# Performance work log

Hardware: AMD Instinct MI355X
Metric: run time of the kernel (lower is better)

## Reference

```python
import jax, jax.numpy as jnp
import numpy as np

B, S, E, H = 4, 1024, 1024, 16
HD = E // H
MAX_SEQ = 5000


def setup_inputs() -> dict:
    key = jax.random.key(0)
    ks = jax.random.split(key, 10)
    def lin(kw, kb):
        w = jax.random.normal(kw, (E, E), dtype=jnp.float32) * (1.0 / np.sqrt(E))
        b = jax.random.normal(kb, (E,), dtype=jnp.float32) * 0.01
        return w, b
    wq, bq = lin(ks[0], ks[1])
    wk, bk = lin(ks[2], ks[3])
    wv, bv = lin(ks[4], ks[5])
    wo, bo = lin(ks[6], ks[7])
    rpe_table = jax.random.normal(ks[8], (H, 2 * MAX_SEQ - 1, HD), dtype=jnp.float32) * 0.02
    x = jax.random.normal(ks[9], (B, S, E), dtype=jnp.float32)
    return {"x": x, "wq": wq, "bq": bq, "wk": wk, "bk": bk,
            "wv": wv, "bv": bv, "wo": wo, "bo": bo, "rpe_table": rpe_table}


def reference(x, wq, bq, wk, bk, wv, bv, wo, bo, rpe_table):
    b, s, e = x.shape
    scale = 1.0 / np.sqrt(HD)
    # projections (torch Linear: y = x @ W^T + b), reshape to (b, h, s, hd)
    q = (x @ wq.T + bq).reshape(b, s, H, HD).transpose(0, 2, 1, 3)
    k = (x @ wk.T + bk).reshape(b, s, H, HD).transpose(0, 2, 1, 3)
    v = (x @ wv.T + bv).reshape(b, s, H, HD).transpose(0, 2, 1, 3)
    scores = jnp.einsum('bhqd,bhkd->bhqk', q, k) * scale
    # RPE: rpe[h, q, k, d] = table[h, q - k + s - 1, d]; factor the einsum:
    # rel[b,h,q,r] = sum_d q[b,h,q,d] * table[h,r,d], then gather r = q - k + s - 1
    table = rpe_table[:, : 2 * s - 1]               # (H, 2s-1, HD)
    rel = jnp.einsum('bhqd,hrd->bhqr', q, table)    # (b, H, s, 2s-1)
    idx = jnp.arange(s)[:, None] - jnp.arange(s)[None, :] + (s - 1)  # (s, s)
    rpe_scores = jnp.take_along_axis(
        rel, jnp.broadcast_to(idx[None, None], (b, H, s, s)), axis=-1)
    attn = jax.nn.softmax(scores + rpe_scores, axis=-1)
    ctx = jnp.einsum('bhqk,bhkd->bhqd', attn, v)
    ctx = ctx.transpose(0, 2, 1, 3).reshape(b, s, e)
    return ctx @ wo.T + bo
```

## Files before the change

kernel.cpp:

```cpp
#include <hip/hip_runtime.h>
#include <hip/hip_bf16.h>
#include <stdint.h>

typedef __attribute__((ext_vector_type(8))) short s8v;
typedef __attribute__((ext_vector_type(4))) float f32x4;
typedef __attribute__((ext_vector_type(16))) float f32x16;

union V16 { uint4 u4; unsigned int u[4]; s8v s; };

__device__ inline s8v u4_to_s8(uint4 v) { V16 c; c.u4 = v; return c.s; }
__device__ inline s8v words_to_s8(unsigned int a, unsigned int b, unsigned int c, unsigned int d) {
  V16 t; t.u[0] = a; t.u[1] = b; t.u[2] = c; t.u[3] = d; return t.s;
}
__device__ inline unsigned short f2b(float f) {
  __hip_bfloat16 h = __float2bfloat16(f);
  unsigned short u; __builtin_memcpy(&u, &h, 2); return u;
}
__device__ inline unsigned int pack2(float lo, float hi) {
  return ((unsigned int)f2b(hi) << 16) | (unsigned int)f2b(lo);
}
__device__ inline unsigned int cvtpk(float lo, float hi) {
  unsigned int r; asm("v_cvt_pk_bf16_f32 %0, %1, %2" : "=v"(r) : "v"(lo), "v"(hi)); return r;
}
__device__ inline float exp2_fast(float x) {
#if __has_builtin(__builtin_amdgcn_exp2f)
  return __builtin_amdgcn_exp2f(x);
#else
  float y; asm("v_exp_f32 %0, %1" : "=v"(y) : "v"(x)); return y;
#endif
}
__device__ inline void gld16(const void* g, void* lds) {
  __builtin_amdgcn_global_load_lds((const __attribute__((address_space(1))) void*)g,
                                   (__attribute__((address_space(3))) void*)lds, 16, 0, 0);
}

#define LOG2E 1.4426950408889634f

__global__ void cvt_fused_kernel(const float* __restrict__ x, const float* __restrict__ wq,
                                 const float* __restrict__ wk, const float* __restrict__ wv,
                                 const float* __restrict__ wo, const float* __restrict__ tb,
                                 __hip_bfloat16* __restrict__ XB, __hip_bfloat16* __restrict__ WQKV,
                                 __hip_bfloat16* __restrict__ WOb, __hip_bfloat16* __restrict__ TBL) {
  const int bid = blockIdx.x;
  if (bid < 4096) {
    size_t i = ((size_t)bid * 256 + threadIdx.x) * 8;
    const float* src; __hip_bfloat16* dst; size_t off;
    if (i < 4194304)      { src = x;  dst = XB;             off = i; }
    else if (i < 5242880) { src = wq; dst = WQKV;           off = i - 4194304; }
    else if (i < 6291456) { src = wk; dst = WQKV + 1048576; off = i - 5242880; }
    else if (i < 7340032) { src = wv; dst = WQKV + 2097152; off = i - 6291456; }
    else                  { src = wo; dst = WOb;            off = i - 7340032; }
    const float4* s4 = (const float4*)(src + off);
    float4 a = s4[0], b = s4[1];
    uint4 o;
    o.x = pack2(a.x, a.y); o.y = pack2(a.z, a.w);
    o.z = pack2(b.x, b.y); o.w = pack2(b.z, b.w);
    *(uint4*)(dst + off) = o;
  } else {
    size_t i = ((size_t)(bid - 4096) * 256 + threadIdx.x) * 8;
    int h = (int)(i >> 17);
    int rem = (int)(i & 131071);
    int r = rem >> 6, c = rem & 63;
    uint4 o;
    if (r < 2047) {
      const float4* s4 = (const float4*)(tb + ((size_t)h * 9999 + r) * 64 + c);
      float4 a = s4[0], b = s4[1];
      o.x = pack2(a.x * LOG2E, a.y * LOG2E); o.y = pack2(a.z * LOG2E, a.w * LOG2E);
      o.z = pack2(b.x * LOG2E, b.y * LOG2E); o.w = pack2(b.z * LOG2E, b.w * LOG2E);
    } else { o.x = 0u; o.y = 0u; o.z = 0u; o.w = 0u; }
    *(uint4*)(TBL + i) = o;
  }
}

__global__ __launch_bounds__(256, 3) void gemm_qkv(
    const __hip_bfloat16* __restrict__ A,
    const __hip_bfloat16* __restrict__ Bt,
    const float* __restrict__ bq, const float* __restrict__ bk, const float* __restrict__ bv,
    __hip_bfloat16* __restrict__ QB, __hip_bfloat16* __restrict__ KB,
    __hip_bfloat16* __restrict__ VTB) {
  __shared__ __align__(16) char smem[32768];
  char* As = smem;
  char* Bs = smem + 16384;
  const int tid = threadIdx.x;
  const int w = tid >> 6, l = tid & 63;
  const int wr = w >> 1, wc = w & 1;
  const int lr = l & 15, lg = l >> 4;
  const int m0 = blockIdx.y * 128, n0 = blockIdx.x * 128;

  f32x4 acc[4][4] = {};

  for (int kt = 0; kt < 16; ++kt) {
    __syncthreads();
    #pragma unroll
    for (int i = 0; i < 4; ++i) {
      const int off = i * 4096 + w * 1024;
      const int loff = off + l * 16;
      const int row = loff >> 7;
      const int cb = loff & 127;
      const int sc = cb ^ ((row & 7) << 4);
      gld16((const char*)A  + (size_t)(m0 + row) * 2048 + kt * 128 + sc, As + off);
      gld16((const char*)Bt + (size_t)(n0 + row) * 2048 + kt * 128 + sc, Bs + off);
    }
    asm volatile("s_waitcnt vmcnt(0)" ::: "memory");
    __syncthreads();
    #pragma unroll
    for (int ks = 0; ks < 2; ++ks) {
      uint4 af[4], bf4[4];
      #pragma unroll
      for (int i = 0; i < 4; ++i) {
        const int ra = wr * 64 + i * 16 + lr;
        const int rb = wc * 64 + i * 16 + lr;
        const int cb = ks * 64 + lg * 16;
        af[i]  = *(const uint4*)(As + ra * 128 + (cb ^ ((ra & 7) << 4)));
        bf4[i] = *(const uint4*)(Bs + rb * 128 + (cb ^ ((rb & 7) << 4)));
      }
      #pragma unroll
      for (int i = 0; i < 4; ++i) {
        #pragma unroll
        for (int j = 0; j < 4; ++j)
          acc[i][j] = __builtin_amdgcn_mfma_f32_16x16x32_bf16(u4_to_s8(af[i]), u4_to_s8(bf4[j]), acc[i][j], 0, 0, 0);
      }
    }
  }

  const int mrow = m0 + wr * 64 + lg * 4;
  const int ncol = n0 + wc * 64 + lr;
  const int cls = blockIdx.x >> 3;

  if (cls < 2) {
    const float sc = cls ? 0.125f * LOG2E : 1.0f;
    const float* bias = cls ? bk : bq;
    __hip_bfloat16* op = cls ? KB : QB;
    #pragma unroll
    for (int j = 0; j < 4; ++j) {
      const int n = ncol - cls * 1024 + j * 16;
      const float bia = bias[n];
      const int hh = n >> 6, hd = n & 63;
      #pragma unroll
      for (int i = 0; i < 4; ++i) {
        #pragma unroll
        for (int r = 0; r < 4; ++r) {
          const int m = mrow + i * 16 + r;
          const int bb = m >> 10, ss = m & 1023;
          op[(((size_t)(bb * 16 + hh)) * 1024 + ss) * 64 + hd] = __float2bfloat16((acc[i][j][r] + bia) * sc);
        }
      }
    }
  } else {
    #pragma unroll
    for (int j = 0; j < 4; ++j) {
      const int f = ncol - 2048 + j * 16;
      const float bia = bv[f];
      const int fh = f >> 6, fd = f & 63;
      #pragma unroll
      for (int i = 0; i < 4; ++i) {
        const int m = mrow + i * 16;
        const int bb = m >> 10, ss = m & 1023;
        ushort4 qv;
        qv.x = f2b(acc[i][j][0] + bia); qv.y = f2b(acc[i][j][1] + bia);
        qv.z = f2b(acc[i][j][2] + bia); qv.w = f2b(acc[i][j][3] + bia);
        *(ushort4*)((char*)VTB + (((size_t)bb * 1048576 + (size_t)fh * 65536 + fd * 1024 + ss) * 2)) = qv;
      }
    }
  }
}

__global__ __launch_bounds__(256, 3) void gemm_out(
    const __hip_bfloat16* __restrict__ A,
    const __hip_bfloat16* __restrict__ Bt,
    const float* __restrict__ bo,
    float* __restrict__ out) {
  __shared__ __align__(16) char smem[32768];
  char* As = smem;
  char* Bs = smem + 16384;
  const int tid = threadIdx.x;
  const int w = tid >> 6, l = tid & 63;
  const int wr = w >> 1, wc = w & 1;
  const int lr = l & 15, lg = l >> 4;
  const int m0 = blockIdx.y * 128, n0 = blockIdx.x * 128;

  f32x4 acc[4][4] = {};

  for (int kt = 0; kt < 16; ++kt) {
    __syncthreads();
    #pragma unroll
    for (int i = 0; i < 4; ++i) {
      const int off = i * 4096 + w * 1024;
      const int loff = off + l * 16;
      const int row = loff >> 7;
      const int cb = loff & 127;
      const int sc = cb ^ ((row & 7) << 4);
      gld16((const char*)A  + (size_t)(m0 + row) * 2048 + kt * 128 + sc, As + off);
      gld16((const char*)Bt + (size_t)(n0 + row) * 2048 + kt * 128 + sc, Bs + off);
    }
    asm volatile("s_waitcnt vmcnt(0)" ::: "memory");
    __syncthreads();
    #pragma unroll
    for (int ks = 0; ks < 2; ++ks) {
      uint4 af[4], bf4[4];
      #pragma unroll
      for (int i = 0; i < 4; ++i) {
        const int ra = wr * 64 + i * 16 + lr;
        const int rb = wc * 64 + i * 16 + lr;
        const int cb = ks * 64 + lg * 16;
        af[i]  = *(const uint4*)(As + ra * 128 + (cb ^ ((ra & 7) << 4)));
        bf4[i] = *(const uint4*)(Bs + rb * 128 + (cb ^ ((rb & 7) << 4)));
      }
      #pragma unroll
      for (int i = 0; i < 4; ++i) {
        #pragma unroll
        for (int j = 0; j < 4; ++j)
          acc[i][j] = __builtin_amdgcn_mfma_f32_16x16x32_bf16(u4_to_s8(af[i]), u4_to_s8(bf4[j]), acc[i][j], 0, 0, 0);
      }
    }
  }

  const int mrow = m0 + wr * 64 + lg * 4;
  const int ncol = n0 + wc * 64 + lr;
  #pragma unroll
  for (int j = 0; j < 4; ++j) {
    const int n = ncol + j * 16;
    const float bia = bo[n];
    #pragma unroll
    for (int i = 0; i < 4; ++i) {
      #pragma unroll
      for (int r = 0; r < 4; ++r) {
        const int m = mrow + i * 16 + r;
        out[(size_t)m * 1024 + n] = acc[i][j][r] + bia;
      }
    }
  }
}

__global__ __launch_bounds__(256, 2) void attn_kernel(
    const __hip_bfloat16* __restrict__ Qg,
    const __hip_bfloat16* __restrict__ Kg,
    const __hip_bfloat16* __restrict__ VTg,
    const __hip_bfloat16* __restrict__ Tg,
    __hip_bfloat16* __restrict__ Cg) {
  __shared__ __align__(16) char smem[65536];
  char* Klds = smem;
  char* Tlds = smem + 8192;
  const int tid = threadIdx.x;
  const int w = tid >> 6, l = tid & 63;
  const int ql = l & 31, half = l >> 5;
  char* relw = smem + 32768 + w * 8192;

  const int bx = blockIdx.x;
  const int work = (bx & 7) * 64 + (bx >> 3);
  const int b = work & 3, hqt = work >> 2;
  const int h = hqt >> 3, qt = hqt & 7;
  const int qb = qt * 128;
  const int q0 = qb + 32 * w;

  const size_t bh = (size_t)(b * 16 + h);
  const char* Qb = (const char*)Qg + bh * 131072;
  const char* Kb = (const char*)Kg + bh * 131072;
  const char* Vb = (const char*)VTg + bh * 131072;
  const char* Tb = (const char*)Tg + (size_t)h * 262144;

  const int relsw = ql * 256 + ((ql & 15) << 4);
  const int u4 = (ql << 2) - (half << 4);
  const int k0sw = ql * 128 + ((ql & 7) << 4);
  const int k1sw = (32 + ql) * 128 + ((ql & 7) << 4);

  auto stageK = [&](int k0n) {
    #pragma unroll
    for (int i = 0; i < 2; ++i) {
      const int loff = i * 4096 + w * 1024 + l * 16;
      const int row = loff >> 7, cb = loff & 127;
      const int sc = cb ^ ((row & 7) << 4);
      gld16(Kb + (size_t)(k0n + row) * 128 + sc, Klds + i * 4096 + w * 1024);
    }
  };
  auto stageT = [&](int rsrc) {
    const int slot = (int)(((unsigned)(rsrc >> 6)) % 3u);
    char* dst = Tlds + slot * 8192;
    #pragma unroll
    for (int i = 0; i < 2; ++i) {
      const int loff = i * 4096 + w * 1024 + l * 16;
      const int row = loff >> 7, cb = loff & 127;
      const int sc = cb ^ ((row & 7) << 4);
      gld16(Tb + (size_t)(rsrc + row) * 128 + sc, dst + i * 4096 + w * 1024);
    }
  };

  s8v qv[4];
  {
    const char* qrow = Qb + (size_t)(q0 + ql) * 128 + half * 16;
    #pragma unroll
    for (int ds = 0; ds < 4; ++ds) qv[ds] = u4_to_s8(*(const uint4*)(qrow + ds * 32));
  }

  f32x16 cacc0 = {}, cacc1 = {};
  f32x16 rcache = {};
  float mL = -1.0e30f, lsum = 0.0f;
  int rbase = qb + 960;

  for (int kt = 0; kt < 16; ++kt, rbase -= 64) {
    __syncthreads();
    stageK(kt * 64);
    stageT(rbase);
    if (kt == 0) { stageT(rbase + 64); stageT(rbase + 128); }
    asm volatile("s_waitcnt vmcnt(0)" ::: "memory");
    __syncthreads();

    uint4 vr[8];
    { const int kn = kt * 128;
      #pragma unroll
      for (int t = 0; t < 2; ++t)
        #pragma unroll
        for (int ks = 0; ks < 4; ++ks)
          vr[t * 4 + ks] = *(const uint4*)(Vb + (size_t)(t * 32 + ql) * 2048 + kn + ks * 32 + half * 16);
    }

    auto relTile = [&](int bt) {
      const int slot = (int)(((unsigned)(rbase >> 6) + (unsigned)((w + bt) >> 1)) % 3u);
      const int rowin = ((w + bt) & 1) * 32 + ql;
      const int tbsw = slot * 8192 + rowin * 128 + ((ql & 7) << 4);
      f32x16 racc = {};
      __builtin_amdgcn_s_setprio(1);
      #pragma unroll
      for (int ds = 0; ds < 4; ++ds) {
        const int cb = ds * 32 + half * 16;
        uint4 tf = *(const uint4*)(Tlds + (tbsw ^ cb));
        racc = __builtin_amdgcn_mfma_f32_32x32x16_bf16(u4_to_s8(tf), qv[ds], racc, 0, 0, 0);
      }
      __builtin_amdgcn_s_setprio(0);
      return racc;
    };

    f32x16 racc2 = (kt == 0) ? relTile(2) : rcache;
    #pragma unroll
    for (int g = 0; g < 4; ++g)
      #pragma unroll
      for (int j = 0; j < 4; ++j) {
        const int pos4 = (u4 + 4 * (-1 - j - 8 * g)) & 124;
        *(float*)(relw + (relsw ^ pos4)) = racc2[4 * g + j];
      }
    f32x16 racc0 = relTile(0);
    #pragma unroll
    for (int g = 0; g < 4; ++g)
      #pragma unroll
      for (int j = 0; j < 4; ++j) {
        const int pos4 = ((u4 + 4 * (63 - j - 8 * g)) & 252) | 128;
        *(float*)(relw + (relsw ^ pos4)) = racc0[4 * g + j];
      }
    rcache = racc0;
    f32x16 racc1 = relTile(1);
    #pragma unroll
    for (int g = 0; g < 4; ++g)
      #pragma unroll
      for (int j = 0; j < 4; ++j) {
        const int pos4 = (u4 + 4 * (31 - j - 8 * g)) & 252;
        *(float*)(relw + (relsw ^ pos4)) = racc1[4 * g + j];
      }

    f32x16 p0 = {}, p1 = {};
    __builtin_amdgcn_s_setprio(1);
    #pragma unroll
    for (int ds = 0; ds < 4; ++ds) {
      const int cb = ds * 32 + half * 16;
      uint4 kf0 = *(const uint4*)(Klds + (k0sw ^ cb));
      uint4 kf1 = *(const uint4*)(Klds + (k1sw ^ cb));
      p0 = __builtin_amdgcn_mfma_f32_32x32x16_bf16(u4_to_s8(kf0), qv[ds], p0, 0, 0, 0);
      p1 = __builtin_amdgcn_mfma_f32_32x32x16_bf16(u4_to_s8(kf1), qv[ds], p1, 0, 0, 0);
    }
    __builtin_amdgcn_s_setprio(0);

    #pragma unroll
    for (int mp = 0; mp < 4; ++mp) {
      const int X0 = 32 * mp + 16 * half;
      f32x4 r0 = *(const f32x4*)(relw + (relsw ^ X0));
      f32x4 r1 = *(const f32x4*)(relw + (relsw ^ (X0 + 128)));
      #pragma unroll
      for (int j = 0; j < 4; ++j) {
        p0[4 * mp + j] += r0[j];
        p1[4 * mp + j] += r1[j];
      }
    }

    float mx[8];
    #pragma unroll
    for (int i = 0; i < 8; ++i)
      mx[i] = fmaxf(fmaxf(p0[2 * i], p0[2 * i + 1]), fmaxf(p1[2 * i], p1[2 * i + 1]));
    float pmax = fmaxf(fmaxf(fmaxf(mx[0], mx[1]), fmaxf(mx[2], mx[3])),
                       fmaxf(fmaxf(mx[4], mx[5]), fmaxf(mx[6], mx[7])));
    pmax = fmaxf(pmax, __shfl_xor(pmax, 32));
    if (!__all(pmax - mL <= 12.0f)) {
      const float mnew = fmaxf(mL, pmax);
      const float corr = exp2_fast(mL - mnew);
      mL = mnew;
      lsum *= corr;
      #pragma unroll
      for (int r = 0; r < 16; ++r) {
        const float cr = __shfl(corr, (r & 3) + 8 * (r >> 2) + 4 * half);
        cacc0[r] *= cr;
        cacc1[r] *= cr;
      }
    }
    #pragma unroll
    for (int r = 0; r < 16; ++r) {
      p0[r] = exp2_fast(p0[r] - mL);
      p1[r] = exp2_fast(p1[r] - mL);
    }
    float sm[8];
    #pragma unroll
    for (int i = 0; i < 8; ++i)
      sm[i] = (p0[2 * i] + p0[2 * i + 1]) + (p1[2 * i] + p1[2 * i + 1]);
    float psum = ((sm[0] + sm[1]) + (sm[2] + sm[3])) + ((sm[4] + sm[5]) + (sm[6] + sm[7]));
    psum += __shfl_xor(psum, 32);
    lsum += psum;

    unsigned int w0[8], w1[8];
    #pragma unroll
    for (int jw = 0; jw < 8; ++jw) {
      w0[jw] = cvtpk(p0[2 * jw], p0[2 * jw + 1]);
      w1[jw] = cvtpk(p1[2 * jw], p1[2 * jw + 1]);
    }
    unsigned int r0x[4], r1x[4];
    #pragma unroll
    for (int i = 0; i < 4; ++i) {
      const int jkeep = (i & 1) + 4 * (i >> 1);
      const int jsend = jkeep + 2;
      unsigned int v0 = half ? w0[jkeep] : w0[jsend];
      unsigned int v1 = half ? w1[jkeep] : w1[jsend];
      r0x[i] = (unsigned int)__shfl_xor((int)v0, 32);
      r1x[i] = (unsigned int)__shfl_xor((int)v1, 32);
    }

    __builtin_amdgcn_s_setprio(1);
    #pragma unroll
    for (int ks = 0; ks < 4; ++ks) {
      const int mm = ks & 1;
      unsigned int f0_, f1_, f2_, f3_;
      if (ks < 2) {
        f0_ = half ? r0x[2 * mm]     : w0[4 * mm];
        f1_ = half ? r0x[2 * mm + 1] : w0[4 * mm + 1];
        f2_ = half ? w0[4 * mm + 2]  : r0x[2 * mm];
        f3_ = half ? w0[4 * mm + 3]  : r0x[2 * mm + 1];
      } else {
        f0_ = half ? r1x[2 * mm]     : w1[4 * mm];
        f1_ = half ? r1x[2 * mm + 1] : w1[4 * mm + 1];
        f2_ = half ? w1[4 * mm + 2]  : r1x[2 * mm];
        f3_ = half ? w1[4 * mm + 3]  : r1x[2 * mm + 1];
      }
      s8v pf = words_to_s8(f0_, f1_, f2_, f3_);
      cacc0 = __builtin_amdgcn_mfma_f32_32x32x16_bf16(pf, u4_to_s8(vr[ks]), cacc0, 0, 0, 0);
      cacc1 = __builtin_amdgcn_mfma_f32_32x32x16_bf16(pf, u4_to_s8(vr[4 + ks]), cacc1, 0, 0, 0);
    }
    __builtin_amdgcn_s_setprio(0);
  }

  #pragma unroll
  for (int r = 0; r < 16; ++r) {
    const int qr = (r & 3) + 8 * (r >> 2) + 4 * half;
    const float inv = 1.0f / __shfl(lsum, qr);
    const size_t row = (size_t)b * 1024 + q0 + qr;
    const size_t basei = row * 1024 + h * 64 + ql;
    Cg[basei]      = __float2bfloat16(cacc0[r] * inv);
    Cg[basei + 32] = __float2bfloat16(cacc1[r] * inv);
  }
}

extern "C" void kernel_launch(void* const* d_in, const int* in_sizes, int n_in,
                              void* d_out, int out_size, void* d_ws, size_t ws_size,
                              hipStream_t stream) {
  (void)in_sizes; (void)n_in; (void)out_size; (void)ws_size;
  const float* x  = (const float*)d_in[0];
  const float* wq = (const float*)d_in[1];
  const float* bq = (const float*)d_in[2];
  const float* wk = (const float*)d_in[3];
  const float* bk = (const float*)d_in[4];
  const float* wv = (const float*)d_in[5];
  const float* bv = (const float*)d_in[6];
  const float* wo = (const float*)d_in[7];
  const float* bo = (const float*)d_in[8];
  const float* tb = (const float*)d_in[9];

  char* ws = (char*)d_ws;
  __hip_bfloat16* XB   = (__hip_bfloat16*)(ws);
  __hip_bfloat16* WQKV = (__hip_bfloat16*)(ws + 8388608);
  __hip_bfloat16* WOb  = (__hip_bfloat16*)(ws + 14680064);
  __hip_bfloat16* TBL  = (__hip_bfloat16*)(ws + 16777216);
  __hip_bfloat16* QB   = (__hip_bfloat16*)(ws + 20971520);
  __hip_bfloat16* KB   = (__hip_bfloat16*)(ws + 29360128);
  __hip_bfloat16* VTB  = (__hip_bfloat16*)(ws + 37748736);
  __hip_bfloat16* CTX  = (__hip_bfloat16*)(ws + 46137344);

  cvt_fused_kernel<<<5120, 256, 0, stream>>>(x, wq, wk, wv, wo, tb, XB, WQKV, WOb, TBL);
  gemm_qkv<<<dim3(24, 32), 256, 0, stream>>>(XB, WQKV, bq, bk, bv, QB, KB, VTB);
  attn_kernel<<<512, 256, 0, stream>>>(QB, KB, VTB, TBL, CTX);
  gemm_out<<<dim3(8, 32), 256, 0, stream>>>(CTX, WOb, bo, (float*)d_out);
}
```

Baseline: 110.1 us.

## Split attention KV loop across two wave groups with split-K softmax merge

Doubles the attention block to 512 threads: two groups of four waves each process alternating 64-key tiles, and their partial max/sum/context results are merged through LDS at the end. The per-iteration LDS staging of K and RPE table tiles is dropped, along with its block-wide barriers. Each wave now reads K and table fragments straight from global memory. The rel-tile cache that reused one tile across iterations is also removed, so every iteration recomputes all three rel tiles, adding MFMA work and direct global loads in exchange for more parallelism and no barriers.

```diff
diff --git a/kernel.cpp b/kernel.cpp
--- a/kernel.cpp
+++ b/kernel.cpp
@@ -232,19 +232,20 @@
   }
 }
 
-__global__ __launch_bounds__(256, 2) void attn_kernel(
+__global__ __launch_bounds__(512, 2) void attn_kernel(
     const __hip_bfloat16* __restrict__ Qg,
     const __hip_bfloat16* __restrict__ Kg,
     const __hip_bfloat16* __restrict__ VTg,
     const __hip_bfloat16* __restrict__ Tg,
     __hip_bfloat16* __restrict__ Cg) {
   __shared__ __align__(16) char smem[65536];
-  char* Klds = smem;
-  char* Tlds = smem + 8192;
   const int tid = threadIdx.x;
-  const int w = tid >> 6, l = tid & 63;
+  const int wall = tid >> 6;
+  const int g = wall >> 2;
+  const int w = wall & 3;
+  const int l = tid & 63;
   const int ql = l & 31, half = l >> 5;
-  char* relw = smem + 32768 + w * 8192;
+  char* relw = smem + wall * 8192;
 
   const int bx = blockIdx.x;
   const int work = (bx & 7) * 64 + (bx >> 3);
@@ -261,29 +262,6 @@
 
   const int relsw = ql * 256 + ((ql & 15) << 4);
   const int u4 = (ql << 2) - (half << 4);
-  const int k0sw = ql * 128 + ((ql & 7) << 4);
-  const int k1sw = (32 + ql) * 128 + ((ql & 7) << 4);
-
-  auto stageK = [&](int k0n) {
-    #pragma unroll
-    for (int i = 0; i < 2; ++i) {
-      const int loff = i * 4096 + w * 1024 + l * 16;
-      const int row = loff >> 7, cb = loff & 127;
-      const int sc = cb ^ ((row & 7) << 4);
-      gld16(Kb + (size_t)(k0n + row) * 128 + sc, Klds + i * 4096 + w * 1024);
-    }
-  };
-  auto stageT = [&](int rsrc) {
-    const int slot = (int)(((unsigned)(rsrc >> 6)) % 3u);
-    char* dst = Tlds + slot * 8192;
-    #pragma unroll
-    for (int i = 0; i < 2; ++i) {
-      const int loff = i * 4096 + w * 1024 + l * 16;
-      const int row = loff >> 7, cb = loff & 127;
-      const int sc = cb ^ ((row & 7) << 4);
-      gld16(Tb + (size_t)(rsrc + row) * 128 + sc, dst + i * 4096 + w * 1024);
-    }
-  };
 
   s8v qv[4];
   {
@@ -293,17 +271,12 @@
   }
 
   f32x16 cacc0 = {}, cacc1 = {};
-  f32x16 rcache = {};
   float mL = -1.0e30f, lsum = 0.0f;
-  int rbase = qb + 960;
-
-  for (int kt = 0; kt < 16; ++kt, rbase -= 64) {
-    __syncthreads();
-    stageK(kt * 64);
-    stageT(rbase);
-    if (kt == 0) { stageT(rbase + 64); stageT(rbase + 128); }
-    asm volatile("s_waitcnt vmcnt(0)" ::: "memory");
-    __syncthreads();
+
+  for (int s = 0; s < 8; ++s) {
+    const int kt = 2 * s + g;
+    const int k0 = kt * 64;
+    const int rbase = qb + 960 - 64 * kt;
 
     uint4 vr[8];
     { const int kn = kt * 128;
@@ -314,59 +287,45 @@
           vr[t * 4 + ks] = *(const uint4*)(Vb + (size_t)(t * 32 + ql) * 2048 + kn + ks * 32 + half * 16);
     }
 
-    auto relTile = [&](int bt) {
-      const int slot = (int)(((unsigned)(rbase >> 6) + (unsigned)((w + bt) >> 1)) % 3u);
-      const int rowin = ((w + bt) & 1) * 32 + ql;
-      const int tbsw = slot * 8192 + rowin * 128 + ((ql & 7) << 4);
+    #pragma unroll
+    for (int ti = 0; ti < 3; ++ti) {
+      const int bt = (ti == 0) ? 2 : ((ti == 1) ? 0 : 1);
+      const char* trow = Tb + (size_t)(rbase + 32 * (w + bt) + ql) * 128 + half * 16;
       f32x16 racc = {};
       __builtin_amdgcn_s_setprio(1);
       #pragma unroll
       for (int ds = 0; ds < 4; ++ds) {
-        const int cb = ds * 32 + half * 16;
-        uint4 tf = *(const uint4*)(Tlds + (tbsw ^ cb));
+        uint4 tf = *(const uint4*)(trow + ds * 32);
         racc = __builtin_amdgcn_mfma_f32_32x32x16_bf16(u4_to_s8(tf), qv[ds], racc, 0, 0, 0);
       }
       __builtin_amdgcn_s_setprio(0);
-      return racc;
-    };
-
-    f32x16 racc2 = (kt == 0) ? relTile(2) : rcache;
-    #pragma unroll
-    for (int g = 0; g < 4; ++g)
-      #pragma unroll
-      for (int j = 0; j < 4; ++j) {
-        const int pos4 = (u4 + 4 * (-1 - j - 8 * g)) & 124;
-        *(float*)(relw + (relsw ^ pos4)) = racc2[4 * g + j];
-      }
-    f32x16 racc0 = relTile(0);
-    #pragma unroll
-    for (int g = 0; g < 4; ++g)
-      #pragma unroll
-      for (int j = 0; j < 4; ++j) {
-        const int pos4 = ((u4 + 4 * (63 - j - 8 * g)) & 252) | 128;
-        *(float*)(relw + (relsw ^ pos4)) = racc0[4 * g + j];
-      }
-    rcache = racc0;
-    f32x16 racc1 = relTile(1);
-    #pragma unroll
-    for (int g = 0; g < 4; ++g)
-      #pragma unroll
-      for (int j = 0; j < 4; ++j) {
-        const int pos4 = (u4 + 4 * (31 - j - 8 * g)) & 252;
-        *(float*)(relw + (relsw ^ pos4)) = racc1[4 * g + j];
-      }
+      #pragma unroll
+      for (int g4 = 0; g4 < 4; ++g4) {
+        #pragma unroll
+        for (int j = 0; j < 4; ++j) {
+          int pos4;
+          if (bt == 2)      pos4 = (u4 + 4 * (-1 - j - 8 * g4)) & 124;
+          else if (bt == 0) pos4 = ((u4 + 4 * (63 - j - 8 * g4)) & 252) | 128;
+          else              pos4 = (u4 + 4 * (31 - j - 8 * g4)) & 252;
+          *(float*)(relw + (relsw ^ pos4)) = racc[4 * g4 + j];
+        }
+      }
+    }
 
     f32x16 p0 = {}, p1 = {};
-    __builtin_amdgcn_s_setprio(1);
-    #pragma unroll
-    for (int ds = 0; ds < 4; ++ds) {
-      const int cb = ds * 32 + half * 16;
-      uint4 kf0 = *(const uint4*)(Klds + (k0sw ^ cb));
-      uint4 kf1 = *(const uint4*)(Klds + (k1sw ^ cb));
-      p0 = __builtin_amdgcn_mfma_f32_32x32x16_bf16(u4_to_s8(kf0), qv[ds], p0, 0, 0, 0);
-      p1 = __builtin_amdgcn_mfma_f32_32x32x16_bf16(u4_to_s8(kf1), qv[ds], p1, 0, 0, 0);
-    }
-    __builtin_amdgcn_s_setprio(0);
+    {
+      const char* krow0 = Kb + (size_t)(k0 + ql) * 128 + half * 16;
+      const char* krow1 = krow0 + 32 * 128;
+      __builtin_amdgcn_s_setprio(1);
+      #pragma unroll
+      for (int ds = 0; ds < 4; ++ds) {
+        uint4 kf0 = *(const uint4*)(krow0 + ds * 32);
+        uint4 kf1 = *(const uint4*)(krow1 + ds * 32);
+        p0 = __builtin_amdgcn_mfma_f32_32x32x16_bf16(u4_to_s8(kf0), qv[ds], p0, 0, 0, 0);
+        p1 = __builtin_amdgcn_mfma_f32_32x32x16_bf16(u4_to_s8(kf1), qv[ds], p1, 0, 0, 0);
+      }
+      __builtin_amdgcn_s_setprio(0);
+    }
 
     #pragma unroll
     for (int mp = 0; mp < 4; ++mp) {
@@ -452,14 +411,45 @@
     __builtin_amdgcn_s_setprio(0);
   }
 
-  #pragma unroll
-  for (int r = 0; r < 16; ++r) {
-    const int qr = (r & 3) + 8 * (r >> 2) + 4 * half;
-    const float inv = 1.0f / __shfl(lsum, qr);
-    const size_t row = (size_t)b * 1024 + q0 + qr;
-    const size_t basei = row * 1024 + h * 64 + ql;
-    Cg[basei]      = __float2bfloat16(cacc0[r] * inv);
-    Cg[basei + 32] = __float2bfloat16(cacc1[r] * inv);
+  __syncthreads();
+  if (g == 1) {
+    char* xch = smem + w * 8192;
+    #pragma unroll
+    for (int c = 0; c < 4; ++c) {
+      f32x4 qa  = {cacc0[4 * c], cacc0[4 * c + 1], cacc0[4 * c + 2], cacc0[4 * c + 3]};
+      f32x4 qb2 = {cacc1[4 * c], cacc1[4 * c + 1], cacc1[4 * c + 2], cacc1[4 * c + 3]};
+      *(f32x4*)(xch + l * 128 + ((c * 16) ^ ((l & 7) << 4))) = qa;
+      *(f32x4*)(xch + l * 128 + (((c + 4) * 16) ^ ((l & 7) << 4))) = qb2;
+    }
+    *(float2*)(smem + 32768 + w * 512 + l * 8) = make_float2(mL, lsum);
+  }
+  __syncthreads();
+  if (g == 0) {
+    const float2 mo = *(const float2*)(smem + 32768 + w * 512 + l * 8);
+    const float mstar = fmaxf(mL, mo.x);
+    const float se = exp2_fast(mL - mstar);
+    const float so = exp2_fast(mo.x - mstar);
+    const float lstar = lsum * se + mo.y * so;
+    const char* xch = smem + w * 8192;
+    f32x4 o0[4], o1[4];
+    #pragma unroll
+    for (int c = 0; c < 4; ++c) {
+      o0[c] = *(const f32x4*)(xch + l * 128 + ((c * 16) ^ ((l & 7) << 4)));
+      o1[c] = *(const f32x4*)(xch + l * 128 + (((c + 4) * 16) ^ ((l & 7) << 4)));
+    }
+    #pragma unroll
+    for (int r = 0; r < 16; ++r) {
+      const int qr = (r & 3) + 8 * (r >> 2) + 4 * half;
+      const float cre = __shfl(se, qr);
+      const float cro = __shfl(so, qr);
+      const float inv = 1.0f / __shfl(lstar, qr);
+      const float v0 = (cacc0[r] * cre + o0[r >> 2][r & 3] * cro) * inv;
+      const float v1 = (cacc1[r] * cre + o1[r >> 2][r & 3] * cro) * inv;
+      const size_t row = (size_t)b * 1024 + q0 + qr;
+      const size_t basei = row * 1024 + h * 64 + ql;
+      Cg[basei]      = __float2bfloat16(v0);
+      Cg[basei + 32] = __float2bfloat16(v1);
+    }
   }
 }
 
@@ -490,6 +480,6 @@
 
   cvt_fused_kernel<<<5120, 256, 0, stream>>>(x, wq, wk, wv, wo, tb, XB, WQKV, WOb, TBL);
   gemm_qkv<<<dim3(24, 32), 256, 0, stream>>>(XB, WQKV, bq, bk, bv, QB, KB, VTB);
-  attn_kernel<<<512, 256, 0, stream>>>(QB, KB, VTB, TBL, CTX);
+  attn_kernel<<<512, 512, 0, stream>>>(QB, KB, VTB, TBL, CTX);
   gemm_out<<<dim3(8, 32), 256, 0, stream>>>(CTX, WOb, bo, (float*)d_out);
 }
```

Measured after the change: 169.1 us. 1.54x slower.
